# Optimization experiments

Hardware: AMD Instinct MI355X
Metric: run time of the kernel (lower is better)

The kernel has to match this reference:

```python
import jax, jax.numpy as jnp
import numpy as np

B, T, N, D = 4, 24, 5000, 64
M, K = 256, 20
TEMP = 0.5
MASK_T = int(T * 0.2)


def _random_walk(A):
    # D^-1 A with inf -> 0, as in calculate_random_walk_matrix
    deg = A.sum(axis=1)
    d_inv = jnp.where(deg > 0, 1.0 / deg, 0.0)
    return d_inv[:, None] * A


def _gnn(h, S1, S2, W, b):
    # SpatialConvOrderK, order=1, support_len=2, include_self=True
    # h: [B, C, N, T]; diffusion along node axis; 1x1 conv == channel matmul
    m1 = jnp.einsum('bcnt,mn->bcmt', h, S1)
    m2 = jnp.einsum('bcnt,mn->bcmt', h, S2)
    hc = jnp.concatenate([h, m1, m2], axis=1)  # [B, 3C, N, T]
    return jnp.einsum('bcnt,cd->bdnt', hc, W) + b[None, :, None, None]


def _encode(x, S1, S2, W_start, b_start, W1, b1, W2, b2):
    h = x @ W_start + b_start                 # [B, T, N, D]
    h = jnp.transpose(h, (0, 3, 2, 1))        # [B, D, N, T]
    h = jax.nn.relu(_gnn(h, S1, S2, W1, b1))
    h = _gnn(h, S1, S2, W2, b2)
    return h                                  # [B, D, N, T]


def _normalize(z):
    # cosine-similarity normalization over channel axis (dim=1), torch eps=1e-8
    n = jnp.sqrt(jnp.sum(z * z, axis=1, keepdims=True))
    return z / jnp.maximum(n, 1e-8)


def _forward(x, adj, W_start, b_start, W1, b1, W2, b2, Wf1, bf1, Wf2, bf2,
             missing_idx, pos_idx, neg_idx):
    S1 = _random_walk(adj)
    S2 = _random_walk(adj.T)
    h_ori = _encode(x, S1, S2, W_start, b_start, W1, b1, W2, b2)
    # augmented view: time-masked input through the same encoder
    x_aug = x.at[:, :MASK_T].set(0.0)
    h_aug = _encode(x_aug, S1, S2, W_start, b_start, W1, b1, W2, b2)
    # imputation head: final_linear1 -> relu -> final_linear2
    ht = jnp.transpose(h_ori, (0, 3, 2, 1))   # [B, T, N, D]
    y = jax.nn.relu(ht @ Wf1 + bf1) @ Wf2 + bf2  # [B, T, N, 1]
    # vectorized RSCL: batched gather + cosine sim + InfoNCE (label 0 = positive)
    Zo = _normalize(jnp.transpose(h_ori, (0, 1, 3, 2)))  # [B, D, T, N]
    Za = _normalize(jnp.transpose(h_aug, (0, 1, 3, 2)))
    anchor = Zo[..., missing_idx]             # [B, D, T, M]
    pos = Za[..., pos_idx]                    # [B, D, T, M]
    neg = Za[..., neg_idx]                    # [B, D, T, M, K]
    pos_sim = jnp.sum(anchor * pos, axis=1)                  # [B, T, M]
    neg_sim = jnp.einsum('bdtm,bdtmk->btmk', anchor, neg)    # [B, T, M, K]
    logits = jnp.concatenate([pos_sim[..., None], neg_sim], axis=-1) / TEMP
    # cross-entropy with label 0 == logsumexp - positive logit
    loss = jnp.mean(jax.nn.logsumexp(logits, axis=-1) - logits[..., 0])
    return y, loss


def setup_inputs() -> dict:
    key = jax.random.key(0)
    ks = jax.random.split(key, 12)
    x = jax.random.normal(ks[0], (B, T, N, 1), jnp.float32)
    adj = jax.random.uniform(ks[1], (N, N), jnp.float32)
    missing_idx = jax.random.randint(ks[2], (M,), 0, N)
    pos_idx = jax.random.randint(ks[3], (M,), 0, N)
    neg_idx = jax.random.randint(ks[4], (M, K), 0, N)
    s = lambda k, shp, fan: (jax.random.normal(k, shp, jnp.float32) / np.sqrt(fan)).astype(jnp.float32)
    W_start = s(ks[5], (1, D), 1.0)
    b_start = jnp.zeros((D,), jnp.float32)
    W1 = s(ks[6], (3 * D, D), 3.0 * D)
    b1 = jnp.zeros((D,), jnp.float32)
    W2 = s(ks[7], (3 * D, D), 3.0 * D)
    b2 = jnp.zeros((D,), jnp.float32)
    Wf1 = s(ks[8], (D, D // 2), float(D))
    bf1 = jnp.zeros((D // 2,), jnp.float32)
    Wf2 = s(ks[9], (D // 2, 1), float(D // 2))
    bf2 = jnp.zeros((1,), jnp.float32)
    return dict(x=x, adj=adj, W_start=W_start, b_start=b_start, W1=W1, b1=b1,
                W2=W2, b2=b2, Wf1=Wf1, bf1=bf1, Wf2=Wf2, bf2=bf2,
                missing_idx=missing_idx, pos_idx=pos_idx, neg_idx=neg_idx)


def reference(x, adj, W_start, b_start, W1, b1, W2, b2, Wf1, bf1, Wf2, bf2,
              missing_idx, pos_idx, neg_idx):
    return _forward(x, adj, W_start, b_start, W1, b1, W2, b2, Wf1, bf1, Wf2, bf2,
                    missing_idx, pos_idx, neg_idx)
```

## Files before the change

kernel.cpp:

```cpp
#include <hip/hip_runtime.h>

typedef unsigned char u8;
typedef unsigned short u16;
typedef unsigned int u32;
typedef __attribute__((ext_vector_type(8))) short short8;
typedef __attribute__((ext_vector_type(8))) u16 u16x8;
typedef __attribute__((ext_vector_type(4))) float f32x4;
typedef __attribute__((ext_vector_type(4))) int i32x4;
typedef __attribute__((ext_vector_type(8))) int i32x8;

#define N_NODES 5000
#define NP 5120
#define BTOT 96
#define J_DIM 6144
#define TT 24
#define KNEG 20

__device__ __forceinline__ float b2f(u16 u){ union{u32 i; float f;} x; x.i = ((u32)u)<<16; return x.f; }
__device__ __forceinline__ u16 f2b(float f){ union{float fl; u32 i;} x; x.fl = f; u32 r = (x.i + 0x7fffu + ((x.i>>16)&1u))>>16; return (u16)r; }
__device__ __forceinline__ u8 f2e4(float f){ return (u8)(__builtin_amdgcn_cvt_pk_fp8_f32(f, 0.f, 0, false) & 0xff); }

#define GPERM(r) ((((r)>>1)&3) | (((r)&1)<<2))
#define GLOAD16(g, l) __builtin_amdgcn_global_load_lds((const __attribute__((address_space(1))) void*)(g), (__attribute__((address_space(3))) void*)(l), 16, 0, 0)

__global__ void k_prep(const float* __restrict__ Ws, const float* __restrict__ bs,
                       const float* __restrict__ W1, const float* __restrict__ b1,
                       const float* __restrict__ W2, const float* __restrict__ b2,
                       float* __restrict__ consts, u16* __restrict__ w2t)
{
  int d = threadIdx.x;
  float u0=0.f,u1=0.f,u2=0.f,bb=0.f;
  for (int c=0;c<64;c++){
    float w = Ws[c];
    float a = W1[c*64+d], b_ = W1[(64+c)*64+d], cw = W1[(128+c)*64+d];
    u0 += w*a; u1 += w*b_; u2 += w*cw;
    bb += bs[c]*(a+b_+cw);
  }
  bb += b1[d];
  consts[d]=u0; consts[64+d]=u1; consts[128+d]=u2; consts[192+d]=bb;
  __shared__ float rb[64];
  rb[d] = fmaxf(bb, 0.f);
  __syncthreads();
  float cA=0.f,cB=0.f,cC=0.f;
  for (int c=0;c<64;c++){
    float r = rb[c];
    cA += r*W2[c*64+d]; cB += r*W2[(64+c)*64+d]; cC += r*W2[(128+c)*64+d];
  }
  consts[256+d]=cA; consts[320+d]=cB; consts[384+d]=cC;
  for (int c=0;c<192;c++) w2t[d*192 + c] = f2b(W2[c*64 + d]);
  __syncthreads();
  float b2v = b2[d];
  for (int vi=0; vi<4; vi++){
    float vv = cA + ((vi&1) ? cB : 0.f) + ((vi&2) ? cC : 0.f) + b2v;
    rb[d] = vv*vv;
    __syncthreads();
    for (int o=32;o;o>>=1){ if (d<o) rb[d]+=rb[d+o]; __syncthreads(); }
    float nrm = sqrtf(rb[0]);
    consts[448 + vi*64 + d] = vv / fmaxf(nrm, 1e-8f);
    __syncthreads();
  }
}

__global__ __launch_bounds__(256) void k_convT(const float* __restrict__ adj,
    u8* __restrict__ abf, u8* __restrict__ atbf,
    float* __restrict__ degr, float* __restrict__ degc)
{
  __shared__ u8 tN[64][80];
  __shared__ u8 tT[64][80];
  __shared__ float rsum[64];
  __shared__ float cpart[16][64];
  const int tid = threadIdx.x;
  const int bx = blockIdx.x, by = blockIdx.y;
  const int c4 = (tid & 15) * 4;
  const int g  = tid >> 4;
  const int gk = bx*64 + c4;
  float ca0=0.f, ca1=0.f, ca2=0.f, ca3=0.f;
  #pragma unroll
  for (int p=0;p<4;p++){
    int r = p*16 + g;
    int gm = by*64 + r;
    float v0=0.f,v1=0.f,v2=0.f,v3=0.f;
    if (gm < N_NODES && gk + 3 < N_NODES){
      const float4 v = *(const float4*)(adj + (size_t)gm*N_NODES + gk);
      v0=v.x; v1=v.y; v2=v.z; v3=v.w;
    }
    u8 p0=f2e4(v0), p1=f2e4(v1), p2=f2e4(v2), p3=f2e4(v3);
    *(u32*)&tN[r][c4] = (u32)p0 | ((u32)p1<<8) | ((u32)p2<<16) | ((u32)p3<<24);
    tT[c4+0][r]=p0; tT[c4+1][r]=p1; tT[c4+2][r]=p2; tT[c4+3][r]=p3;
    float ls = v0+v1+v2+v3;
    ls += __shfl_xor(ls,1); ls += __shfl_xor(ls,2);
    ls += __shfl_xor(ls,4); ls += __shfl_xor(ls,8);
    if ((tid & 15) == 0) rsum[r] = ls;
    ca0+=v0; ca1+=v1; ca2+=v2; ca3+=v3;
  }
  cpart[g][c4+0]=ca0; cpart[g][c4+1]=ca1; cpart[g][c4+2]=ca2; cpart[g][c4+3]=ca3;
  __syncthreads();
  if (tid < 64){
    int gm = by*64 + tid;
    if (gm < N_NODES && rsum[tid] != 0.f) atomicAdd(&degr[gm], rsum[tid]);
    float cs = 0.f;
    #pragma unroll
    for (int gg=0;gg<16;gg++) cs += cpart[gg][tid];
    int gc = bx*64 + tid;
    if (gc < N_NODES && cs != 0.f) atomicAdd(&degc[gc], cs);
  }
  const int j = tid >> 2, c16 = (tid & 3) * 16;
  *(i32x4*)(abf  + (size_t)(by*64+j)*NP + bx*64 + c16) = *(const i32x4*)(&tN[j][c16]);
  *(i32x4*)(atbf + (size_t)(bx*64+j)*NP + by*64 + c16) = *(const i32x4*)(&tT[j][c16]);
}

__global__ void k_xbf(const float* __restrict__ x, u8* __restrict__ xbf){
  int i4 = (blockIdx.x*256 + threadIdx.x)*4;
  int j = i4 / NP, n = i4 - j*NP;
  u32 w = 0;
  if (j < BTOT){
    #pragma unroll
    for (int e=0;e<4;e++){
      float v = (n+e < N_NODES) ? x[(size_t)j*N_NODES + n + e] : 0.f;
      w |= ((u32)f2e4(v)) << (8*e);
    }
  }
  *(u32*)(xbf + i4) = w;
}

__device__ __forceinline__ i32x8 frag8(const u8* lds, int row, int kb2){
  int g = GPERM(row & 7);
  int ba = row*128 + ((kb2 ^ g)<<4);
  union { i32x8 v; i32x4 h[2]; } f;
  f.h[0] = *(const i32x4*)(lds + ba);
  f.h[1] = *(const i32x4*)(lds + (ba^16));
  return f.v;
}

__global__ __launch_bounds__(256) void k_sgemm8(const u8* __restrict__ abf,
    const u8* __restrict__ atbf, const u8* __restrict__ B,
    float* __restrict__ y1sl, float* __restrict__ y2sl)
{
  __shared__ __align__(16) u8 lA[128*128];
  __shared__ __align__(16) u8 lB[128*128];
  const u8* A = blockIdx.z ? atbf : abf;
  float* ysl = blockIdx.z ? y2sl : y1sl;
  const int tid = threadIdx.x, lane = tid & 63, wv = tid >> 6;
  const int wm = (wv >> 1) * 64, wj = (wv & 1) * 64;
  const int m0 = blockIdx.x * 128;
  const int kbase = blockIdx.y * 640;
  f32x4 acc[4][4] = {};
  const int q = tid >> 3;
  const int sc = ((tid & 7) ^ GPERM(q & 7)) << 4;
  const u8* gA = A + (size_t)(m0 + q)*NP + kbase + sc;
  const u8* gB = B + (size_t)q*NP + kbase + sc;
  for (int k0 = 0; k0 < 640; k0 += 128) {
    #pragma unroll
    for (int s=0;s<4;s++){
      GLOAD16(gA + (size_t)(s*32)*NP + k0, (char*)lA + s*4096 + wv*1024);
      GLOAD16(gB + (size_t)(s*32)*NP + k0, (char*)lB + s*4096 + wv*1024);
    }
    __syncthreads();
    i32x8 af[4], bfv[4];
    const int kb2 = (lane >> 4) * 2;
    #pragma unroll
    for (int i=0;i<4;i++){
      af[i]  = frag8(lA, wm + i*16 + (lane&15), kb2);
      bfv[i] = frag8(lB, wj + i*16 + (lane&15), kb2);
    }
    #pragma unroll
    for (int i=0;i<4;i++)
      #pragma unroll
      for (int j=0;j<4;j++)
        acc[i][j] = __builtin_amdgcn_mfma_scale_f32_16x16x128_f8f6f4(
            af[i], bfv[j], acc[i][j], 0, 0, 0, 0x7f7f7f7f, 0, 0x7f7f7f7f);
    __syncthreads();
  }
  float* yb = ysl + (size_t)blockIdx.y * NP * 128;
  #pragma unroll
  for (int i=0;i<4;i++)
    #pragma unroll
    for (int r=0;r<4;r++){
      int row = m0 + wm + i*16 + (lane>>4)*4 + r;
      #pragma unroll
      for (int j=0;j<4;j++){
        int col = wj + j*16 + (lane&15);
        yb[(size_t)row*128 + col] = acc[i][j][r];
      }
    }
}

__global__ __launch_bounds__(256) void k_yred(const float* __restrict__ y1sl,
    const float* __restrict__ y2sl, const float* __restrict__ degr,
    const float* __restrict__ degc, float* __restrict__ y1r, float* __restrict__ y2r)
{
  __shared__ float tb[128][66];
  const int n0 = blockIdx.x*64;
  const int bt = threadIdx.x & 127, nh = threadIdx.x >> 7;
  const int nl = threadIdx.x & 63, bh = threadIdx.x >> 6;
  #pragma unroll 4
  for (int k=0;k<32;k++){
    int n = nh*32 + k;
    float s = 0.f;
    #pragma unroll
    for (int sl=0; sl<8; sl++) s += y1sl[((size_t)sl*NP + n0+n)*128 + bt];
    tb[bt][n] = s;
  }
  __syncthreads();
  {
    float dv = degr[n0+nl];
    float iv = (dv > 0.f) ? 1.f/dv : 0.f;
    #pragma unroll 4
    for (int b=0;b<32;b++){
      int btw = bh*32 + b;
      y1r[(size_t)btw*NP + n0 + nl] = iv * tb[btw][nl];
    }
  }
  __syncthreads();
  #pragma unroll 4
  for (int k=0;k<32;k++){
    int n = nh*32 + k;
    float s = 0.f;
    #pragma unroll
    for (int sl=0; sl<8; sl++) s += y2sl[((size_t)sl*NP + n0+n)*128 + bt];
    tb[bt][n] = s;
  }
  __syncthreads();
  {
    float dv = degc[n0+nl];
    float iv = (dv > 0.f) ? 1.f/dv : 0.f;
    #pragma unroll 4
    for (int b=0;b<32;b++){
      int btw = bh*32 + b;
      y2r[(size_t)btw*NP + n0 + nl] = iv * tb[btw][nl];
    }
  }
}

__global__ __launch_bounds__(256) void k_h1(const float* __restrict__ x,
    const float* __restrict__ y1r, const float* __restrict__ y2r,
    const float* __restrict__ consts, u8* __restrict__ h1t, u16* __restrict__ h1n)
{
  __shared__ u8 trT[64][80];
  const int tid = threadIdx.x;
  const int n = tid & 63, d0 = (tid >> 6) * 16;
  const int n0 = blockIdx.x * 64;
  const int bt = blockIdx.y;
  const int gn = n0 + n;
  const bool valid = gn < N_NODES;
  float xv  = valid ? x[(size_t)bt*N_NODES + gn] : 0.f;
  float y1s = y1r[(size_t)bt*NP + gn];
  float y2s = y2r[(size_t)bt*NP + gn];
  float hv[16];
  #pragma unroll
  for (int e=0;e<16;e++){
    int d = d0 + e;
    float v = 0.f;
    if (valid)
      v = fmaxf(xv*consts[d] + y1s*consts[64+d] + y2s*consts[128+d] + consts[192+d], 0.f);
    hv[e] = v;
    trT[d][n] = f2e4(v);
  }
  u16x8 p0, p1;
  #pragma unroll
  for (int e=0;e<8;e++){ p0[e]=f2b(hv[e]); p1[e]=f2b(hv[8+e]); }
  u16* dst = h1n + (size_t)gn*J_DIM + bt*64 + d0;
  *(u16x8*)dst = p0;
  *(u16x8*)(dst+8) = p1;
  __syncthreads();
  const int d = tid >> 2, c16 = (tid & 3) * 16;
  *(i32x4*)(h1t + (size_t)(bt*64+d)*NP + n0 + c16) = *(const i32x4*)(&trT[d][c16]);
}

__global__ __launch_bounds__(256) void k_gemm8(
    const u8* __restrict__ abf, const u8* __restrict__ atbf,
    const u8* __restrict__ Bt, u16* __restrict__ Pb, u16* __restrict__ Qb,
    const float* __restrict__ degr, const float* __restrict__ degc)
{
  __shared__ __align__(16) u8 lA[128*128];
  __shared__ __align__(16) u8 lB[128*128];
  const u8* A = blockIdx.z ? atbf : abf;
  u16* C = blockIdx.z ? Qb : Pb;
  const float* dg = blockIdx.z ? degc : degr;
  const int tid = threadIdx.x, lane = tid & 63, wv = tid >> 6;
  const int wm = (wv >> 1) * 64, wj = (wv & 1) * 64;
  const int m0 = blockIdx.x * 128;
  const int j0 = blockIdx.y * 128;
  f32x4 acc[4][4] = {};
  const int q = tid >> 3;
  const int sc = ((tid & 7) ^ GPERM(q & 7)) << 4;
  const u8* gA = A + (size_t)(m0 + q)*NP + sc;
  const u8* gB = Bt + (size_t)(j0 + q)*NP + sc;
  for (int k0 = 0; k0 < NP; k0 += 128) {
    #pragma unroll
    for (int s=0;s<4;s++){
      GLOAD16(gA + (size_t)(s*32)*NP + k0, (char*)lA + s*4096 + wv*1024);
      GLOAD16(gB + (size_t)(s*32)*NP + k0, (char*)lB + s*4096 + wv*1024);
    }
    __syncthreads();
    i32x8 af[4], bfv[4];
    const int kb2 = (lane >> 4) * 2;
    #pragma unroll
    for (int i=0;i<4;i++){
      af[i]  = frag8(lA, wm + i*16 + (lane&15), kb2);
      bfv[i] = frag8(lB, wj + i*16 + (lane&15), kb2);
    }
    #pragma unroll
    for (int i=0;i<4;i++)
      #pragma unroll
      for (int j=0;j<4;j++)
        acc[i][j] = __builtin_amdgcn_mfma_scale_f32_16x16x128_f8f6f4(
            af[i], bfv[j], acc[i][j], 0, 0, 0, 0x7f7f7f7f, 0, 0x7f7f7f7f);
    __syncthreads();
  }
  #pragma unroll
  for (int i=0;i<4;i++)
    #pragma unroll
    for (int r=0;r<4;r++){
      int row = m0 + wm + i*16 + (lane>>4)*4 + r;
      float dv = dg[row];
      float scl = (dv > 0.f) ? 1.f/dv : 0.f;
      #pragma unroll
      for (int j=0;j<4;j++){
        int col = j0 + wj + j*16 + (lane&15);
        C[(size_t)row*J_DIM + col] = f2b(acc[i][j][r] * scl);
      }
    }
}

__global__ __launch_bounds__(256) void k_comb(const u16* __restrict__ h1n,
  const u16* __restrict__ P, const u16* __restrict__ Q,
  const u16* __restrict__ w2t, const float* __restrict__ b2,
  const float* __restrict__ Wf1, const float* __restrict__ bf1,
  const float* __restrict__ Wf2, const float* __restrict__ bf2,
  u16* __restrict__ horin, float* __restrict__ yout)
{
  __shared__ float w1L[64*33];
  __shared__ float hT[64][65];
  __shared__ float b1L[32], w2Ls[32];
  const int tid = threadIdx.x;
  for (int i = tid; i < 2048; i += 256) w1L[(i>>5)*33 + (i&31)] = Wf1[i];
  if (tid < 32){ b1L[tid] = bf1[tid]; w2Ls[tid] = Wf2[tid]; }
  const int lane = tid & 63;
  const int wv = tid >> 6;
  const int n0 = blockIdx.x * 64 + wv * 16;
  const int bt = blockIdx.y;
  const int rl = lane & 15, kh = lane >> 4;

  f32x4 acc[4] = {};
  const size_t rowoff = (size_t)(n0 + rl) * J_DIM + bt*64;
  const u16* bases[3] = { h1n + rowoff, P + rowoff, Q + rowoff };
  #pragma unroll
  for (int s=0;s<3;s++){
    const u16* base = bases[s];
    #pragma unroll
    for (int kk=0;kk<2;kk++){
      short8 af = *(const short8*)(base + kk*32 + kh*8);
      #pragma unroll
      for (int j=0;j<4;j++){
        short8 bf = *(const short8*)(w2t + (j*16+rl)*192 + s*64 + kk*32 + kh*8);
        acc[j] = __builtin_amdgcn_mfma_f32_16x16x32_bf16(af, bf, acc[j], 0,0,0);
      }
    }
  }
  float hvv[4][4];
  #pragma unroll
  for (int j=0;j<4;j++){
    float bias = b2[j*16 + rl];
    #pragma unroll
    for (int r=0;r<4;r++) hvv[j][r] = acc[j][r] + bias;
  }
  float inv[4];
  #pragma unroll
  for (int r=0;r<4;r++){
    float s = hvv[0][r]*hvv[0][r] + hvv[1][r]*hvv[1][r]
            + hvv[2][r]*hvv[2][r] + hvv[3][r]*hvv[3][r];
    s += __shfl_xor(s,1); s += __shfl_xor(s,2);
    s += __shfl_xor(s,4); s += __shfl_xor(s,8);
    inv[r] = 1.f / fmaxf(sqrtf(s), 1e-8f);
  }
  #pragma unroll
  for (int j=0;j<4;j++){
    int d = j*16 + rl;
    #pragma unroll
    for (int r=0;r<4;r++){
      int nn = n0 + kh*4 + r;
      hT[wv*16 + kh*4 + r][d] = hvv[j][r];
      if (nn < N_NODES)
        horin[((size_t)bt*N_NODES + nn)*64 + d] = f2b(hvv[j][r] * inv[r]);
    }
  }
  __syncthreads();
  const int q = tid & 3, node = tid >> 2;
  float h[16];
  #pragma unroll
  for (int e=0;e<16;e++) h[e] = hT[node][q*16 + e];
  float yacc = 0.f;
  #pragma unroll
  for (int jj=0; jj<32; jj++){
    float s = 0.f;
    #pragma unroll
    for (int dl=0; dl<16; dl++) s += h[dl]*w1L[(q*16+dl)*33 + jj];
    s += __shfl_xor(s, 1);
    s += __shfl_xor(s, 2);
    s += b1L[jj];
    yacc += fmaxf(s, 0.f)*w2Ls[jj];
  }
  int gn = blockIdx.x*64 + node;
  if (q == 0 && gn < N_NODES)
    yout[(size_t)bt*N_NODES + gn] = yacc + bf2[0];
}

__global__ __launch_bounds__(256) void k_loss(const u16* __restrict__ horin,
  const int* __restrict__ missing, const int* __restrict__ posi, const int* __restrict__ negi,
  const float* __restrict__ degr, const float* __restrict__ degc,
  const float* __restrict__ consts, float* __restrict__ out)
{
  const int lane = threadIdx.x & 63;
  const int wv = threadIdx.x >> 6;
  const int wg = blockIdx.x*4 + wv;
  const int m = wg & 255;
  const int bt = wg >> 8;
  const bool early = (bt % TT) < 4;

  int na = missing[m];
  float va = b2f(horin[((size_t)bt*N_NODES + na)*64 + lane]);

  float lk[KNEG+1];
  #pragma unroll
  for (int k=0;k<=KNEG;k++){
    int node = (k==0) ? posi[m] : negi[m*KNEG + (k-1)];
    float v;
    if (!early) v = b2f(horin[((size_t)bt*N_NODES + node)*64 + lane]);
    else {
      int vi = (degr[node] > 0.f ? 1 : 0) + (degc[node] > 0.f ? 2 : 0);
      v = consts[448 + vi*64 + lane];
    }
    float dp = va*v;
    #pragma unroll
    for (int o=32;o;o>>=1) dp += __shfl_xor(dp, o);
    lk[k] = dp * 2.f;
  }
  float mx = lk[0];
  #pragma unroll
  for (int k=1;k<=KNEG;k++) mx = fmaxf(mx, lk[k]);
  float se = 0.f;
  #pragma unroll
  for (int k=0;k<=KNEG;k++) se += expf(lk[k]-mx);
  float term = logf(se) + mx - lk[0];
  __shared__ float red[4];
  if (lane == 0) red[wv] = term;
  __syncthreads();
  if (threadIdx.x == 0)
    atomicAdd(out + 480000, (red[0]+red[1]+red[2]+red[3]) * (1.f/24576.f));
}

extern "C" void kernel_launch(void* const* d_in, const int* in_sizes, int n_in,
                              void* d_out, int out_size, void* d_ws, size_t ws_size,
                              hipStream_t stream)
{
  const float* x   = (const float*)d_in[0];
  const float* adj = (const float*)d_in[1];
  const float* Ws  = (const float*)d_in[2];
  const float* bs  = (const float*)d_in[3];
  const float* W1  = (const float*)d_in[4];
  const float* b1  = (const float*)d_in[5];
  const float* W2  = (const float*)d_in[6];
  const float* b2  = (const float*)d_in[7];
  const float* Wf1 = (const float*)d_in[8];
  const float* bf1 = (const float*)d_in[9];
  const float* Wf2 = (const float*)d_in[10];
  const float* bf2 = (const float*)d_in[11];
  const int* missing = (const int*)d_in[12];
  const int* posi    = (const int*)d_in[13];
  const int* negi    = (const int*)d_in[14];
  float* out = (float*)d_out;

  char* w = (char*)d_ws;
  u8*  abf   = (u8*) (w + 0);
  u8*  atbf  = (u8*) (w + 26214400);
  u8*  h1t   = (u8*) (w + 52428800);
  u16* h1n   = (u16*)(w + 83886080);
  u16* Pb    = (u16*)(w + 146800640);
  u16* Qb    = (u16*)(w + 209715200);
  u8*  xbf   = (u8*) (w + 272629760);
  float* degr = (float*)(w + 273285120);
  float* degc = (float*)(w + 273305600);
  float* consts = (float*)(w + 273326080);
  u16* w2t   = (u16*)(w + 273330176);
  u16*   horin = (u16*)(w + 0);
  float* y1sl  = (float*)(w + 146800640);
  float* y2sl  = (float*)(w + 167772160);
  float* y1r   = (float*)(w + 209715200);
  float* y2r   = (float*)(w + 212336640);

  hipMemsetAsync(degr, 0, 40960, stream);
  hipMemsetAsync(out + 480000, 0, 4, stream);

  k_prep<<<1, 64, 0, stream>>>(Ws, bs, W1, b1, W2, b2, consts, w2t);
  k_convT<<<dim3(80,80), 256, 0, stream>>>(adj, abf, atbf, degr, degc);
  k_xbf<<<640, 256, 0, stream>>>(x, xbf);
  k_sgemm8<<<dim3(40,8,2), 256, 0, stream>>>(abf, atbf, xbf, y1sl, y2sl);
  k_yred<<<80, 256, 0, stream>>>(y1sl, y2sl, degr, degc, y1r, y2r);
  k_h1<<<dim3(80,96), 256, 0, stream>>>(x, y1r, y2r, consts, h1t, h1n);
  k_gemm8<<<dim3(40,48,2), 256, 0, stream>>>(abf, atbf, h1t, Pb, Qb, degr, degc);
  k_comb<<<dim3(80,96), 256, 0, stream>>>(h1n, Pb, Qb, w2t, b2, Wf1, bf1, Wf2, bf2, horin, out);
  k_loss<<<6144, 256, 0, stream>>>(horin, missing, posi, negi, degr, degc, consts, out);
}
```

Before: 734.4 us.

## Double-buffer LDS tiles in fp8 GEMM with prefetch two stages ahead

The fp8 MFMA GEMM now uses two LDS buffers per operand and issues the global-to-LDS loads for tile t+2 while tile t is being computed. Explicit vmcnt waits and raw barriers replace the per-iteration __syncthreads pair, and s_setprio raises wave priority around the MFMA block. The aim is to hide global load latency behind matrix math. The cost is twice the LDS per block (64KB), which may lower occupancy. A variable in the head kernel is renamed, with no behavioural effect.

```diff
diff --git a/kernel.cpp b/kernel.cpp
--- a/kernel.cpp
+++ b/kernel.cpp
@@ -272,8 +272,8 @@
     const u8* __restrict__ Bt, u16* __restrict__ Pb, u16* __restrict__ Qb,
     const float* __restrict__ degr, const float* __restrict__ degc)
 {
-  __shared__ __align__(16) u8 lA[128*128];
-  __shared__ __align__(16) u8 lB[128*128];
+  __shared__ __align__(16) u8 lA[2][16384];
+  __shared__ __align__(16) u8 lB[2][16384];
   const u8* A = blockIdx.z ? atbf : abf;
   u16* C = blockIdx.z ? Qb : Pb;
   const float* dg = blockIdx.z ? degc : degr;
@@ -286,28 +286,54 @@
   const int sc = ((tid & 7) ^ GPERM(q & 7)) << 4;
   const u8* gA = A + (size_t)(m0 + q)*NP + sc;
   const u8* gB = Bt + (size_t)(j0 + q)*NP + sc;
-  for (int k0 = 0; k0 < NP; k0 += 128) {
-    #pragma unroll
-    for (int s=0;s<4;s++){
-      GLOAD16(gA + (size_t)(s*32)*NP + k0, (char*)lA + s*4096 + wv*1024);
-      GLOAD16(gB + (size_t)(s*32)*NP + k0, (char*)lB + s*4096 + wv*1024);
-    }
-    __syncthreads();
+
+  #define STAGE8(k0, bufA, bufB) do { \
+    _Pragma("unroll") \
+    for (int s=0;s<4;s++){ \
+      GLOAD16(gA + (size_t)(s*32)*NP + (k0), (char*)(bufA) + s*4096 + wv*1024); \
+      GLOAD16(gB + (size_t)(s*32)*NP + (k0), (char*)(bufB) + s*4096 + wv*1024); \
+    } \
+  } while(0)
+
+  STAGE8(0,   lA[0], lB[0]);
+  STAGE8(128, lA[1], lB[1]);
+  asm volatile("s_waitcnt vmcnt(8)" ::: "memory");
+  __builtin_amdgcn_s_barrier();
+  __builtin_amdgcn_sched_barrier(0);
+
+  const int NT = NP/128;
+  for (int t = 0; t < NT; t++) {
+    const int cur = t & 1;
+    const u8* bA = lA[cur];
+    const u8* bB = lB[cur];
     i32x8 af[4], bfv[4];
     const int kb2 = (lane >> 4) * 2;
     #pragma unroll
     for (int i=0;i<4;i++){
-      af[i]  = frag8(lA, wm + i*16 + (lane&15), kb2);
-      bfv[i] = frag8(lB, wj + i*16 + (lane&15), kb2);
-    }
+      af[i]  = frag8(bA, wm + i*16 + (lane&15), kb2);
+      bfv[i] = frag8(bB, wj + i*16 + (lane&15), kb2);
+    }
+    __builtin_amdgcn_s_setprio(1);
     #pragma unroll
     for (int i=0;i<4;i++)
       #pragma unroll
       for (int j=0;j<4;j++)
         acc[i][j] = __builtin_amdgcn_mfma_scale_f32_16x16x128_f8f6f4(
             af[i], bfv[j], acc[i][j], 0, 0, 0, 0x7f7f7f7f, 0, 0x7f7f7f7f);
-    __syncthreads();
-  }
+    __builtin_amdgcn_s_setprio(0);
+    __builtin_amdgcn_s_barrier();
+    __builtin_amdgcn_sched_barrier(0);
+    if (t + 2 < NT) {
+      STAGE8((t+2)*128, lA[cur], lB[cur]);
+      asm volatile("s_waitcnt vmcnt(8)" ::: "memory");
+    } else {
+      asm volatile("s_waitcnt vmcnt(0)" ::: "memory");
+    }
+    __builtin_amdgcn_s_barrier();
+    __builtin_amdgcn_sched_barrier(0);
+  }
+  #undef STAGE8
+
   #pragma unroll
   for (int i=0;i<4;i++)
     #pragma unroll
@@ -386,23 +412,23 @@
     }
   }
   __syncthreads();
-  const int q = tid & 3, node = tid >> 2;
+  const int qd = tid & 3, node = tid >> 2;
   float h[16];
   #pragma unroll
-  for (int e=0;e<16;e++) h[e] = hT[node][q*16 + e];
+  for (int e=0;e<16;e++) h[e] = hT[node][qd*16 + e];
   float yacc = 0.f;
   #pragma unroll
   for (int jj=0; jj<32; jj++){
     float s = 0.f;
     #pragma unroll
-    for (int dl=0; dl<16; dl++) s += h[dl]*w1L[(q*16+dl)*33 + jj];
+    for (int dl=0; dl<16; dl++) s += h[dl]*w1L[(qd*16+dl)*33 + jj];
     s += __shfl_xor(s, 1);
     s += __shfl_xor(s, 2);
     s += b1L[jj];
     yacc += fmaxf(s, 0.f)*w2Ls[jj];
   }
   int gn = blockIdx.x*64 + node;
-  if (q == 0 && gn < N_NODES)
+  if (qd == 0 && gn < N_NODES)
     yout[(size_t)bt*N_NODES + gn] = yacc + bf2[0];
 }
 
```

Result: faster. 672.3 us (-8.5%).
